# Performance work log

Measured on AMD Instinct MI355X. Metric: run time of the kernel, lower is better.

## Reference

```python
import jax, jax.numpy as jnp
import numpy as np

DIM_HEADS = 64
NB_FEATURES = 256
KERNEL_EPS = 1e-4


def _gaussian_orthogonal_random_matrix(nb_rows, nb_cols, seed=0):
    # scaling == 1: rows scaled by sqrt(nb_cols); orthogonal QR blocks
    rng = np.random.RandomState(seed)
    nb_full_blocks = nb_rows // nb_cols
    blocks = []
    for _ in range(nb_full_blocks):
        unstructured = rng.randn(nb_cols, nb_cols)
        q, _ = np.linalg.qr(unstructured)
        blocks.append(q.T)
    rem = nb_rows - nb_full_blocks * nb_cols
    if rem > 0:
        unstructured = rng.randn(nb_cols, nb_cols)
        q, _ = np.linalg.qr(unstructured)
        blocks.append(q.T[:rem])
    final = np.concatenate(blocks, axis=0)
    multiplier = np.sqrt(float(nb_cols)) * np.ones((nb_rows,))
    return (multiplier[:, None] * final).astype(np.float32)


def setup_inputs() -> dict:
    key = jax.random.key(0)
    kq, kk, kv = jax.random.split(key, 3)
    b, h, n, d = 4, 16, 4096, DIM_HEADS
    q = jax.random.normal(kq, (b, h, n, d), dtype=jnp.float32)
    k = jax.random.normal(kk, (b, h, n, d), dtype=jnp.float32)
    v = jax.random.normal(kv, (b, h, n, d), dtype=jnp.float32)
    proj = jnp.asarray(_gaussian_orthogonal_random_matrix(NB_FEATURES, d))  # [m, d]
    return {"q": q, "k": k, "v": v, "proj": proj}


def _softmax_kernel(data, proj, is_query, eps=KERNEL_EPS):
    d = data.shape[-1]
    m = proj.shape[0]
    data_normalizer = d ** (-0.25)
    ratio = m ** (-0.5)
    # [b,h,n,m]
    data_dash = jnp.einsum('bhnd,md->bhnm', data_normalizer * data, proj)
    diag_data = jnp.sum(data ** 2, axis=-1, keepdims=True) * 0.5 * data_normalizer ** 2
    if is_query:
        stab = jax.lax.stop_gradient(jnp.max(data_dash, axis=-1, keepdims=True))
    else:
        stab = jax.lax.stop_gradient(jnp.max(data_dash, axis=(-1, -2), keepdims=True))
    return ratio * (jnp.exp(data_dash - diag_data - stab) + eps)


def _linear_attention(q, k, v):
    # q,k: [b,h,n,m] features; v: [b,h,n,e]
    k_cumsum = jnp.sum(k, axis=-2)                               # [b,h,m]
    D_inv = 1.0 / jnp.einsum('bhnm,bhm->bhn', q, k_cumsum)       # [b,h,n]
    context = jnp.einsum('bhnm,bhne->bhme', k, v)                # [b,h,m,e]
    return jnp.einsum('bhme,bhnm,bhn->bhne', context, q, D_inv)  # [b,h,n,e]


def reference(q, k, v, proj):
    q_prime = _softmax_kernel(q, proj, is_query=True)
    k_prime = _softmax_kernel(k, proj, is_query=False)
    return _linear_attention(q_prime, k_prime, v)
```

## Files before the change

### kernel.cpp

```cpp
#include <hip/hip_runtime.h>

#define SEQ 4096
#define CDN 0.35355339059327379f
#define DIAGC 0.0625f
#define KEPS 1e-4f

typedef _Float16 f16;
typedef f16 f16x8 __attribute__((ext_vector_type(8)));
typedef f16 f16x4 __attribute__((ext_vector_type(4)));
typedef float f32x4 __attribute__((ext_vector_type(4)));

#define MFMA16(a, b, c) __builtin_amdgcn_mfma_f32_16x16x32_f16(a, b, c, 0, 0, 0)

#define PSTR 72

__device__ __forceinline__ void stage_proj(const float* __restrict__ proj, f16* plds) {
  int t = threadIdx.x;
  int mrow = t >> 2;
  int cb = (t & 3) * 16;
#pragma unroll
  for (int p = 0; p < 4; ++p) {
    int m = mrow + p * 64;
    const float4* src = (const float4*)(proj + m * 64 + cb);
    f16* dst = plds + m * PSTR + cb;
#pragma unroll
    for (int i = 0; i < 4; ++i) {
      float4 v = src[i];
      f16x4 h = {(f16)v.x, (f16)v.y, (f16)v.z, (f16)v.w};
      *(f16x4*)(dst + i * 4) = h;
    }
  }
}

__device__ __forceinline__ f16x8 proj_frag(const f16* plds, int mtile, int ks, int lane) {
  int m = (lane & 15) + 16 * mtile;
  return *(const f16x8*)(plds + m * PSTR + ks * 32 + (lane >> 4) * 8);
}

__device__ __forceinline__ f16x8 pfrag32s(const float* __restrict__ proj, int mt, int ks, int lane) {
  const float4* p = (const float4*)(proj + (size_t)(16 * mt + (lane & 15)) * 64 + ks * 32 + (lane >> 4) * 8);
  float4 a = p[0], b = p[1];
  f16x8 r = {(f16)(a.x*CDN), (f16)(a.y*CDN), (f16)(a.z*CDN), (f16)(a.w*CDN),
             (f16)(b.x*CDN), (f16)(b.y*CDN), (f16)(b.z*CDN), (f16)(b.w*CDN)};
  return r;
}

__device__ __forceinline__ f16x8 row_frag(const float* __restrict__ base, int lane, int ks, float& sq) {
  const float4* p = (const float4*)(base + (size_t)(lane & 15) * 64 + ks * 32 + (lane >> 4) * 8);
  float4 a = p[0], b = p[1];
  sq += a.x*a.x + a.y*a.y + a.z*a.z + a.w*a.w + b.x*b.x + b.y*b.y + b.z*b.z + b.w*b.w;
  f16x8 r = {(f16)(a.x*CDN), (f16)(a.y*CDN), (f16)(a.z*CDN), (f16)(a.w*CDN),
             (f16)(b.x*CDN), (f16)(b.y*CDN), (f16)(b.z*CDN), (f16)(b.w*CDN)};
  return r;
}

#define KSTR 72

__device__ __forceinline__ void stage_kv(const float* __restrict__ kbh,
                                         const float* __restrict__ vbh,
                                         int n0, f16* ktb, f16* vtb,
                                         float* diagb, int t) {
  int r = t >> 3;
  int c8 = (t & 7) * 8;
  const float4* kp = (const float4*)(kbh + (size_t)(n0 + r) * 64 + c8);
  float4 a = kp[0], b = kp[1];
  float sq = a.x*a.x + a.y*a.y + a.z*a.z + a.w*a.w + b.x*b.x + b.y*b.y + b.z*b.z + b.w*b.w;
  f16x8 h = {(f16)a.x, (f16)a.y, (f16)a.z, (f16)a.w,
             (f16)b.x, (f16)b.y, (f16)b.z, (f16)b.w};
  *(f16x8*)(ktb + r * KSTR + c8) = h;
  sq += __shfl_xor(sq, 1, 64);
  sq += __shfl_xor(sq, 2, 64);
  sq += __shfl_xor(sq, 4, 64);
  if ((t & 7) == 0) diagb[r] = sq * DIAGC;
  int nl = t & 63, e8 = (t >> 6) * 8;
  const float4* vp = (const float4*)(vbh + (size_t)(n0 + nl) * 64 + e8);
  float4 va = vp[0], vb = vp[1];
  vtb[(e8 + 0) * KSTR + nl] = (f16)va.x;
  vtb[(e8 + 1) * KSTR + nl] = (f16)va.y;
  vtb[(e8 + 2) * KSTR + nl] = (f16)va.z;
  vtb[(e8 + 3) * KSTR + nl] = (f16)va.w;
  vtb[(e8 + 4) * KSTR + nl] = (f16)vb.x;
  vtb[(e8 + 5) * KSTR + nl] = (f16)vb.y;
  vtb[(e8 + 6) * KSTR + nl] = (f16)vb.z;
  vtb[(e8 + 7) * KSTR + nl] = (f16)vb.w;
}

__global__ __launch_bounds__(512, 4) void k2_ctx(
    const float* __restrict__ kk, const float* __restrict__ vv,
    const float* __restrict__ proj,
    float* __restrict__ ctx_part, float* __restrict__ kcum_part,
    float* __restrict__ stabm, float* __restrict__ vs_part) {
  __shared__ __align__(16) f16 kt[2][64 * KSTR];
  __shared__ __align__(16) f16 vt[2][64 * KSTR];
  __shared__ __align__(16) f16 pht[8][16 * 40];
  __shared__ float diag_all[2][64];
  __shared__ float red2[4][16];
  __shared__ float stabs[8];
  int bh = blockIdx.x & 63, rest = blockIdx.x >> 6;
  int mc = rest & 3, ns = rest >> 2;
  int t = threadIdx.x;
  int w = t >> 6, lane = t & 63;
  int q4 = lane >> 4, l15 = lane & 15;
  int mtl = w & 3, nsub = w >> 2;
  f16x8 pa0 = pfrag32s(proj, mc * 4 + mtl, 0, lane);
  f16x8 pa1 = pfrag32s(proj, mc * 4 + mtl, 1, lane);
  const float* kbh = kk + (size_t)bh * SEQ * 64;
  const float* vbh = vv + (size_t)bh * SEQ * 64;
  f32x4 actx[4];
  f32x4 akc = {0.f, 0.f, 0.f, 0.f};
#pragma unroll
  for (int i = 0; i < 4; ++i) actx[i] = (f32x4){0.f, 0.f, 0.f, 0.f};
  float vsacc[4] = {0.f, 0.f, 0.f, 0.f};
  float M = -1e30f;
  f16x8 ones = {(f16)1.f, (f16)1.f, (f16)1.f, (f16)1.f,
                (f16)1.f, (f16)1.f, (f16)1.f, (f16)1.f};
  int nbase = ns * 1024;
  stage_kv(kbh, vbh, nbase, &kt[0][0], &vt[0][0], &diag_all[0][0], t);
  __syncthreads();
#pragma unroll 1
  for (int it = 0; it < 16; ++it) {
    int n0 = nbase + it * 64;
    int cur = it & 1;
    if (it < 15)
      stage_kv(kbh, vbh, n0 + 64, &kt[cur ^ 1][0], &vt[cur ^ 1][0], &diag_all[cur ^ 1][0], t);
    const f16* ktc = &kt[cur][0];
    const f16* vcur = &vt[cur][0];
    f16x8 ak[2][2];
#pragma unroll
    for (int nt = 0; nt < 2; ++nt) {
      ak[nt][0] = *(const f16x8*)(ktc + (nsub * 32 + nt * 16 + l15) * KSTR + q4 * 8);
      ak[nt][1] = *(const f16x8*)(ktc + (nsub * 32 + nt * 16 + l15) * KSTR + 32 + q4 * 8);
    }
    f32x4 accv[2];
#pragma unroll
    for (int nt = 0; nt < 2; ++nt) {
      f32x4 a = {0.f, 0.f, 0.f, 0.f};
      a = MFMA16(ak[nt][0], pa0, a);
      a = MFMA16(ak[nt][1], pa1, a);
      accv[nt] = a;
    }
    float tm = fmaxf(fmaxf(fmaxf(accv[0][0], accv[0][1]), fmaxf(accv[0][2], accv[0][3])),
                     fmaxf(fmaxf(accv[1][0], accv[1][1]), fmaxf(accv[1][2], accv[1][3])));
#pragma unroll
    for (int m = 1; m < 64; m <<= 1) tm = fmaxf(tm, __shfl_xor(tm, m, 64));
    if (tm > M) {
      float rs = __expf(M - tm);
      akc *= rs;
#pragma unroll
      for (int et = 0; et < 4; ++et) actx[et] *= rs;
      M = tm;
    }
#pragma unroll
    for (int nt = 0; nt < 2; ++nt) {
      float4 dgv = ((const float4*)&diag_all[cur][0])[nsub * 8 + nt * 4 + q4];
      f16x4 ph;
      ph[0] = (f16)__expf(accv[nt][0] - dgv.x - M);
      ph[1] = (f16)__expf(accv[nt][1] - dgv.y - M);
      ph[2] = (f16)__expf(accv[nt][2] - dgv.z - M);
      ph[3] = (f16)__expf(accv[nt][3] - dgv.w - M);
      *(f16x4*)(&pht[w][l15 * 40 + nt * 16 + q4 * 4]) = ph;
    }
    f16x8 bv[4];
#pragma unroll
    for (int et = 0; et < 4; ++et)
      bv[et] = *(const f16x8*)(vcur + (l15 + 16 * et) * KSTR + nsub * 32 + q4 * 8);
    if (mc == 0 && mtl == 0) {
#pragma unroll
      for (int et = 0; et < 4; ++et) {
        float s = 0.f;
#pragma unroll
        for (int j = 0; j < 8; ++j) s += (float)bv[et][j];
        vsacc[et] += s;
      }
    }
    f16x8 aph = *(const f16x8*)(&pht[w][l15 * 40 + q4 * 8]);
    akc = MFMA16(aph, ones, akc);
#pragma unroll
    for (int et = 0; et < 4; ++et) actx[et] = MFMA16(aph, bv[et], actx[et]);
    __syncthreads();
  }
  if (lane == 0) stabs[w] = M;
  __syncthreads();
  float Mp = stabs[w ^ 4];
  float Mt = fmaxf(M, Mp);
  {
    float sc = __expf(M - Mt);
    akc *= sc;
#pragma unroll
    for (int et = 0; et < 4; ++et) actx[et] *= sc;
  }
  if (mc == 0 && mtl == 0) {
#pragma unroll
    for (int et = 0; et < 4; ++et) {
      float s = vsacc[et];
      s += __shfl_xor(s, 16, 64);
      s += __shfl_xor(s, 32, 64);
      if (lane < 16)
        vs_part[(size_t)bh * 512 + (ns * 2 + nsub) * 64 + lane + 16 * et] = s;
    }
  }
  float* red = (float*)&kt[0][0];
  if (nsub == 1) {
#pragma unroll
    for (int et = 0; et < 4; ++et)
#pragma unroll
      for (int r = 0; r < 4; ++r)
        red[mtl * 1024 + (q4 * 4 + r) * 64 + l15 + 16 * et] = actx[et][r];
    if (l15 == 0) {
#pragma unroll
      for (int r = 0; r < 4; ++r) red2[mtl][q4 * 4 + r] = akc[r];
    }
  }
  __syncthreads();
  if (nsub == 0) {
    float* cp = ctx_part + (((size_t)bh * 4 + ns) * 256 + mc * 64 + mtl * 16) * 64;
#pragma unroll
    for (int et = 0; et < 4; ++et)
#pragma unroll
      for (int r = 0; r < 4; ++r)
        cp[(size_t)(q4 * 4 + r) * 64 + l15 + 16 * et] =
            actx[et][r] + red[mtl * 1024 + (q4 * 4 + r) * 64 + l15 + 16 * et];
    if (l15 == 0) {
#pragma unroll
      for (int r = 0; r < 4; ++r)
        kcum_part[((size_t)bh * 4 + ns) * 256 + mc * 64 + mtl * 16 + q4 * 4 + r] =
            akc[r] + red2[mtl][q4 * 4 + r];
    }
    if (lane == 0) stabm[(size_t)bh * 64 + ns * 16 + mc * 4 + mtl] = Mt;
  }
}

__global__ __launch_bounds__(256) void k2c_red(
    const float* __restrict__ ctx_part, const float* __restrict__ kcum_part,
    const float* __restrict__ stabm, const float* __restrict__ vs_part,
    float* __restrict__ ws_kcum, f16* __restrict__ ws_ctxT) {
  __shared__ float tile[64 * 65];
  __shared__ float sred[64];
  __shared__ float vsum_l[64];
  __shared__ float fac[4][4];
  int bh = blockIdx.x & 63, mq = blockIdx.x >> 6;
  int t = threadIdx.x;
  if (t < 64) {
    sred[t] = stabm[(size_t)bh * 64 + t];
    float vs = 0.f;
#pragma unroll
    for (int i = 0; i < 8; ++i) vs += vs_part[(size_t)bh * 512 + i * 64 + t];
    vsum_l[t] = vs;
  }
  __syncthreads();
  float S = -1e30f;
#pragma unroll
  for (int i = 0; i < 64; ++i) S = fmaxf(S, sred[i]);
  if (t < 16) fac[t >> 2][t & 3] = __expf(sred[(t >> 2) * 16 + mq * 4 + (t & 3)] - S);
  __syncthreads();
  const float* cp = ctx_part + ((size_t)bh * 4 * 256 + mq * 64) * 64;
#pragma unroll
  for (int i = 0; i < 16; ++i) {
    int idx = t + i * 256;
    int ml = idx >> 6, e = idx & 63;
    int tl = ml >> 4;
    float acc = KEPS * vsum_l[e];
#pragma unroll
    for (int ns = 0; ns < 4; ++ns)
      acc += fac[ns][tl] * cp[(size_t)ns * 16384 + idx];
    tile[ml * 65 + e] = acc;
  }
  if (t < 64) {
    int tl = t >> 4;
    float acc = KEPS * 4096.f;
#pragma unroll
    for (int ns = 0; ns < 4; ++ns)
      acc += fac[ns][tl] * kcum_part[((size_t)bh * 4 + ns) * 256 + mq * 64 + t];
    ws_kcum[bh * 256 + mq * 64 + t] = acc;
  }
  __syncthreads();
  f16* ct = ws_ctxT + (size_t)bh * 16384 + mq * 64;
  int mj = t & 63, eg = t >> 6;
#pragma unroll
  for (int i = 0; i < 16; ++i) {
    int e = eg + i * 4;
    ct[(size_t)e * 256 + mj] = (f16)tile[mj * 65 + e];
  }
}

#define CSTR 264

__global__ __launch_bounds__(256, 2) void k3_out(
    const float* __restrict__ qq, const float* __restrict__ proj,
    const float* __restrict__ ws_kcum, const f16* __restrict__ ws_ctxT,
    float* __restrict__ out) {
  __shared__ __align__(16) f16 plds[256 * PSTR];
  __shared__ __align__(16) f16 ctx_l[64 * CSTR];
  __shared__ __align__(16) f16 phq[4][16 * 72];
  __shared__ __align__(16) float kcl[256];
  int bh = blockIdx.x >> 4, blk = blockIdx.x & 15;
  int t = threadIdx.x;
  stage_proj(proj, plds);
  kcl[t] = ws_kcum[bh * 256 + t];
  {
    const f16* cb = ws_ctxT + (size_t)bh * 16384;
#pragma unroll
    for (int i = 0; i < 8; ++i) {
      int c = t + i * 256;
      int e = c >> 5, mo = (c & 31) * 8;
      *(f16x8*)(ctx_l + e * CSTR + mo) = *(const f16x8*)(cb + e * 256 + mo);
    }
  }
  int w = t >> 6, lane = t & 63;
  int q4 = lane >> 4, l15 = lane & 15;
  const float* qbh = qq + (size_t)bh * SEQ * 64;
  float* obh = out + (size_t)bh * SEQ * 64;
  __syncthreads();
#pragma unroll 1
  for (int it = 0; it < 4; ++it) {
    int n0 = blk * 256 + w * 64 + it * 16;
    float sq = 0.f;
    f16x8 bq0 = row_frag(qbh + (size_t)n0 * 64, lane, 0, sq);
    f16x8 bq1 = row_frag(qbh + (size_t)n0 * 64, lane, 1, sq);
    sq += __shfl_xor(sq, 16, 64);
    sq += __shfl_xor(sq, 32, 64);
    float diag = sq * DIAGC;
    float st = -1e30f;
#pragma unroll
    for (int mt = 0; mt < 16; ++mt) {
      f32x4 acc = {0.f, 0.f, 0.f, 0.f};
      acc = MFMA16(proj_frag(plds, mt, 0, lane), bq0, acc);
      acc = MFMA16(proj_frag(plds, mt, 1, lane), bq1, acc);
      st = fmaxf(st, fmaxf(fmaxf(acc[0], acc[1]), fmaxf(acc[2], acc[3])));
    }
    st = fmaxf(st, __shfl_xor(st, 16, 64));
    st = fmaxf(st, __shfl_xor(st, 32, 64));
    float dacc = 0.f;
    f32x4 ao[4];
#pragma unroll
    for (int r = 0; r < 4; ++r) ao[r] = (f32x4){0.f, 0.f, 0.f, 0.f};
#pragma unroll
    for (int qtr = 0; qtr < 4; ++qtr) {
#pragma unroll
      for (int m2 = 0; m2 < 4; ++m2) {
        int mt = qtr * 4 + m2;
        f32x4 acc = {0.f, 0.f, 0.f, 0.f};
        acc = MFMA16(proj_frag(plds, mt, 0, lane), bq0, acc);
        acc = MFMA16(proj_frag(plds, mt, 1, lane), bq1, acc);
        float4 kc = ((const float4*)kcl)[mt * 4 + q4];
        float e0 = __expf(acc[0] - diag - st) + KEPS;
        float e1 = __expf(acc[1] - diag - st) + KEPS;
        float e2 = __expf(acc[2] - diag - st) + KEPS;
        float e3 = __expf(acc[3] - diag - st) + KEPS;
        dacc += e0 * kc.x + e1 * kc.y + e2 * kc.z + e3 * kc.w;
        f16x4 ph;
        ph[0] = (f16)e0; ph[1] = (f16)e1; ph[2] = (f16)e2; ph[3] = (f16)e3;
        *(f16x4*)(&phq[w][l15 * 72 + m2 * 16 + q4 * 4]) = ph;
      }
#pragma unroll
      for (int kl = 0; kl < 2; ++kl) {
        int ks2 = qtr * 2 + kl;
        f16x8 bph = *(const f16x8*)(&phq[w][l15 * 72 + kl * 32 + q4 * 8]);
#pragma unroll
        for (int rte = 0; rte < 4; ++rte) {
          f16x8 act = *(const f16x8*)(ctx_l + (l15 + 16 * rte) * CSTR + ks2 * 32 + q4 * 8);
          ao[rte] = MFMA16(act, bph, ao[rte]);
        }
      }
    }
    dacc += __shfl_xor(dacc, 16, 64);
    dacc += __shfl_xor(dacc, 32, 64);
    float dinv = 1.0f / dacc;
#pragma unroll
    for (int rte = 0; rte < 4; ++rte) {
      f32x4 o = ao[rte] * dinv;
      __builtin_nontemporal_store(o, (f32x4*)(obh + (size_t)(n0 + l15) * 64 + rte * 16 + q4 * 4));
    }
  }
}

extern "C" void kernel_launch(void* const* d_in, const int* in_sizes, int n_in,
                              void* d_out, int out_size, void* d_ws, size_t ws_size,
                              hipStream_t stream) {
  const float* q = (const float*)d_in[0];
  const float* k = (const float*)d_in[1];
  const float* v = (const float*)d_in[2];
  const float* proj = (const float*)d_in[3];
  float* out = (float*)d_out;
  float* ws = (float*)d_ws;
  float* ws_kcum = ws + 1024;
  f16*   ws_ctxT = (f16*)(ws + 17408);
  float* ctx_part  = out;
  float* kcum_part = out + 4194304;
  float* stabm     = out + 4259840;
  float* vs_part   = out + 4263936;
  k2_ctx<<<1024, 512, 0, stream>>>(k, v, proj, ctx_part, kcum_part, stabm, vs_part);
  k2c_red<<<256, 256, 0, stream>>>(ctx_part, kcum_part, stabm, vs_part, ws_kcum, ws_ctxT);
  k3_out<<<1024, 256, 0, stream>>>(q, proj, ws_kcum, ws_ctxT, out);
}
```

Measured before the change: 396.2 us.

## Prefetch K/V and Q tiles into registers and halve k3 grid

In k2_ctx the next K/V tile is now loaded into registers at the top of each iteration and only converted and written to shared memory after the MFMA work, so global load latency overlaps compute. In k3_out each block now handles 512 rows instead of 256 (grid 512 instead of 1024), which amortizes the proj/context staging over more rows. It also register-prefetches the next 16 Q rows while the current ones are processed. The cost is more live registers, which may hurt occupancy, and fewer blocks in the output kernel.

```diff
diff --git a/kernel.cpp b/kernel.cpp
--- a/kernel.cpp
+++ b/kernel.cpp
@@ -40,15 +40,6 @@
 __device__ __forceinline__ f16x8 pfrag32s(const float* __restrict__ proj, int mt, int ks, int lane) {
   const float4* p = (const float4*)(proj + (size_t)(16 * mt + (lane & 15)) * 64 + ks * 32 + (lane >> 4) * 8);
   float4 a = p[0], b = p[1];
-  f16x8 r = {(f16)(a.x*CDN), (f16)(a.y*CDN), (f16)(a.z*CDN), (f16)(a.w*CDN),
-             (f16)(b.x*CDN), (f16)(b.y*CDN), (f16)(b.z*CDN), (f16)(b.w*CDN)};
-  return r;
-}
-
-__device__ __forceinline__ f16x8 row_frag(const float* __restrict__ base, int lane, int ks, float& sq) {
-  const float4* p = (const float4*)(base + (size_t)(lane & 15) * 64 + ks * 32 + (lane >> 4) * 8);
-  float4 a = p[0], b = p[1];
-  sq += a.x*a.x + a.y*a.y + a.z*a.z + a.w*a.w + b.x*b.x + b.y*b.y + b.z*b.z + b.w*b.w;
   f16x8 r = {(f16)(a.x*CDN), (f16)(a.y*CDN), (f16)(a.z*CDN), (f16)(a.w*CDN),
              (f16)(b.x*CDN), (f16)(b.y*CDN), (f16)(b.z*CDN), (f16)(b.w*CDN)};
   return r;
@@ -115,14 +106,21 @@
   f16x8 ones = {(f16)1.f, (f16)1.f, (f16)1.f, (f16)1.f,
                 (f16)1.f, (f16)1.f, (f16)1.f, (f16)1.f};
   int nbase = ns * 1024;
+  int sr = t >> 3, sc8 = (t & 7) * 8;
+  int snl = t & 63, se8 = (t >> 6) * 8;
   stage_kv(kbh, vbh, nbase, &kt[0][0], &vt[0][0], &diag_all[0][0], t);
   __syncthreads();
 #pragma unroll 1
   for (int it = 0; it < 16; ++it) {
     int n0 = nbase + it * 64;
     int cur = it & 1;
-    if (it < 15)
-      stage_kv(kbh, vbh, n0 + 64, &kt[cur ^ 1][0], &vt[cur ^ 1][0], &diag_all[cur ^ 1][0], t);
+    float4 pka, pkb, pva, pvb;
+    if (it < 15) {
+      const float4* kp = (const float4*)(kbh + (size_t)(n0 + 64 + sr) * 64 + sc8);
+      pka = kp[0]; pkb = kp[1];
+      const float4* vp = (const float4*)(vbh + (size_t)(n0 + 64 + snl) * 64 + se8);
+      pva = vp[0]; pvb = vp[1];
+    }
     const f16* ktc = &kt[cur][0];
     const f16* vcur = &vt[cur][0];
     f16x8 ak[2][2];
@@ -177,6 +175,27 @@
     akc = MFMA16(aph, ones, akc);
 #pragma unroll
     for (int et = 0; et < 4; ++et) actx[et] = MFMA16(aph, bv[et], actx[et]);
+    if (it < 15) {
+      f16* ktb = &kt[cur ^ 1][0];
+      f16* vtb = &vt[cur ^ 1][0];
+      float sq = pka.x*pka.x + pka.y*pka.y + pka.z*pka.z + pka.w*pka.w +
+                 pkb.x*pkb.x + pkb.y*pkb.y + pkb.z*pkb.z + pkb.w*pkb.w;
+      f16x8 h = {(f16)pka.x, (f16)pka.y, (f16)pka.z, (f16)pka.w,
+                 (f16)pkb.x, (f16)pkb.y, (f16)pkb.z, (f16)pkb.w};
+      *(f16x8*)(ktb + sr * KSTR + sc8) = h;
+      sq += __shfl_xor(sq, 1, 64);
+      sq += __shfl_xor(sq, 2, 64);
+      sq += __shfl_xor(sq, 4, 64);
+      if ((t & 7) == 0) diag_all[cur ^ 1][sr] = sq * DIAGC;
+      vtb[(se8 + 0) * KSTR + snl] = (f16)pva.x;
+      vtb[(se8 + 1) * KSTR + snl] = (f16)pva.y;
+      vtb[(se8 + 2) * KSTR + snl] = (f16)pva.z;
+      vtb[(se8 + 3) * KSTR + snl] = (f16)pva.w;
+      vtb[(se8 + 4) * KSTR + snl] = (f16)pvb.x;
+      vtb[(se8 + 5) * KSTR + snl] = (f16)pvb.y;
+      vtb[(se8 + 6) * KSTR + snl] = (f16)pvb.z;
+      vtb[(se8 + 7) * KSTR + snl] = (f16)pvb.w;
+    }
     __syncthreads();
   }
   if (lane == 0) stabs[w] = M;
@@ -293,8 +312,20 @@
   __shared__ __align__(16) f16 ctx_l[64 * CSTR];
   __shared__ __align__(16) f16 phq[4][16 * 72];
   __shared__ __align__(16) float kcl[256];
-  int bh = blockIdx.x >> 4, blk = blockIdx.x & 15;
+  int bh = blockIdx.x >> 3, blk = blockIdx.x & 7;
   int t = threadIdx.x;
+  int w = t >> 6, lane = t & 63;
+  int q4 = lane >> 4, l15 = lane & 15;
+  const float* qbh = qq + (size_t)bh * SEQ * 64;
+  int nw0 = blk * 512 + w * 128;
+  float4 ca0, cb0, ca1, cb1;
+  {
+    const float* qr = qbh + (size_t)(nw0 + l15) * 64 + q4 * 8;
+    ca0 = ((const float4*)qr)[0];
+    cb0 = ((const float4*)qr)[1];
+    ca1 = ((const float4*)(qr + 32))[0];
+    cb1 = ((const float4*)(qr + 32))[1];
+  }
   stage_proj(proj, plds);
   kcl[t] = ws_kcum[bh * 256 + t];
   {
@@ -306,20 +337,30 @@
       *(f16x8*)(ctx_l + e * CSTR + mo) = *(const f16x8*)(cb + e * 256 + mo);
     }
   }
-  int w = t >> 6, lane = t & 63;
-  int q4 = lane >> 4, l15 = lane & 15;
-  const float* qbh = qq + (size_t)bh * SEQ * 64;
   float* obh = out + (size_t)bh * SEQ * 64;
   __syncthreads();
 #pragma unroll 1
-  for (int it = 0; it < 4; ++it) {
-    int n0 = blk * 256 + w * 64 + it * 16;
-    float sq = 0.f;
-    f16x8 bq0 = row_frag(qbh + (size_t)n0 * 64, lane, 0, sq);
-    f16x8 bq1 = row_frag(qbh + (size_t)n0 * 64, lane, 1, sq);
+  for (int it = 0; it < 8; ++it) {
+    int n0 = nw0 + it * 16;
+    float sq = ca0.x*ca0.x + ca0.y*ca0.y + ca0.z*ca0.z + ca0.w*ca0.w +
+               cb0.x*cb0.x + cb0.y*cb0.y + cb0.z*cb0.z + cb0.w*cb0.w +
+               ca1.x*ca1.x + ca1.y*ca1.y + ca1.z*ca1.z + ca1.w*ca1.w +
+               cb1.x*cb1.x + cb1.y*cb1.y + cb1.z*cb1.z + cb1.w*cb1.w;
+    f16x8 bq0 = {(f16)(ca0.x*CDN), (f16)(ca0.y*CDN), (f16)(ca0.z*CDN), (f16)(ca0.w*CDN),
+                 (f16)(cb0.x*CDN), (f16)(cb0.y*CDN), (f16)(cb0.z*CDN), (f16)(cb0.w*CDN)};
+    f16x8 bq1 = {(f16)(ca1.x*CDN), (f16)(ca1.y*CDN), (f16)(ca1.z*CDN), (f16)(ca1.w*CDN),
+                 (f16)(cb1.x*CDN), (f16)(cb1.y*CDN), (f16)(cb1.z*CDN), (f16)(cb1.w*CDN)};
     sq += __shfl_xor(sq, 16, 64);
     sq += __shfl_xor(sq, 32, 64);
     float diag = sq * DIAGC;
+    float4 na0, nb0, na1, nb1;
+    if (it < 7) {
+      const float* qn = qbh + (size_t)(n0 + 16 + l15) * 64 + q4 * 8;
+      na0 = ((const float4*)qn)[0];
+      nb0 = ((const float4*)qn)[1];
+      na1 = ((const float4*)(qn + 32))[0];
+      nb1 = ((const float4*)(qn + 32))[1];
+    }
     float st = -1e30f;
 #pragma unroll
     for (int mt = 0; mt < 16; ++mt) {
@@ -371,6 +412,7 @@
       f32x4 o = ao[rte] * dinv;
       __builtin_nontemporal_store(o, (f32x4*)(obh + (size_t)(n0 + l15) * 64 + rte * 16 + q4 * 4));
     }
+    if (it < 7) { ca0 = na0; cb0 = nb0; ca1 = na1; cb1 = nb1; }
   }
 }
 
@@ -391,5 +433,5 @@
   float* vs_part   = out + 4263936;
   k2_ctx<<<1024, 512, 0, stream>>>(k, v, proj, ctx_part, kcum_part, stabm, vs_part);
   k2c_red<<<256, 256, 0, stream>>>(ctx_part, kcum_part, stabm, vs_part, ws_kcum, ws_ctxT);
-  k3_out<<<1024, 256, 0, stream>>>(q, proj, ws_kcum, ws_ctxT, out);
-}
+  k3_out<<<512, 256, 0, stream>>>(q, proj, ws_kcum, ws_ctxT, out);
+}
```

After: 387.3 us. 2.2% less time.
